# Kernel optimization log

Measured on AMD Instinct MI355X. Metric: run time of the kernel, lower is better.

## Reference

```python
import jax, jax.numpy as jnp
import numpy as np

B, L, S, H, E = 4, 1024, 1024, 8, 64


def setup_inputs() -> dict:
    key = jax.random.key(0)
    ks = jax.random.split(key, 8)
    return {
        "query": jax.random.normal(ks[0], (B, L, H, E), dtype=jnp.float32),
        "key": jax.random.normal(ks[1], (B, S, H, E), dtype=jnp.float32),
        "value": jax.random.normal(ks[2], (B, S, H, E), dtype=jnp.float32),
        "phi": jax.random.normal(ks[3], (H, L, S), dtype=jnp.float32),
        "log_gain": jnp.asarray(np.log(10.0), dtype=jnp.float32),
        "log_tau": jnp.asarray(np.log(2.0), dtype=jnp.float32),
        "log_tau_comm": jnp.asarray(np.log(0.2), dtype=jnp.float32),
        "hard_mask": jax.random.uniform(ks[4], (L, S), dtype=jnp.float32),
        "u": jax.random.uniform(ks[5], (H, L, S), dtype=jnp.float32),
        "mask_miss_k": jnp.ones((B, S), dtype=jnp.float32),
        "mask_miss_q": jnp.ones((B, L), dtype=jnp.float32),
        "pos": jnp.zeros((B, L), dtype=jnp.float32),
        "causal_mask": 0,
    }


def reference(query, key, value, phi, log_gain, log_tau, log_tau_comm,
              hard_mask, u, mask_miss_k, mask_miss_q, pos, causal_mask):
    # mask_miss_k/q, pos, causal_mask are unused by LieAttention.forward (torch parity)
    E_dim = query.shape[-1]
    scale = 1.0 / float(np.sqrt(E_dim))
    # raw scores (B, H, L, S)
    scores = jnp.einsum('blhe,bshe->bhls', query, key)
    # antisymmetric communication term
    comm = scores - jnp.swapaxes(scores, -1, -2)
    gain = jnp.clip(jnp.exp(log_gain), 1e-3, 1000.0)      # max_gain = 1000
    tau_comm = jnp.clip(jnp.exp(log_tau_comm), 1e-3, 10.0)
    comm_amp = jnp.tanh((gain / tau_comm) * comm)
    att = scale * jax.nn.gelu(comm_amp, approximate=False)  # torch F.gelu = exact erf
    # Gumbel-sigmoid relaxed DAG mask, broadcast over batch: M (1, H, L, S)
    tau = jnp.clip(jnp.exp(log_tau), 0.1, 5.0)             # tau_min/tau_max
    m_relaxed = jax.nn.sigmoid((jnp.log(u + 1e-8) - jnp.log(1.0 - u + 1e-8) + phi) / tau)
    att = att * m_relaxed[None]
    # hard mask (L, S) -> (1, 1, L, S)
    att = att * hard_mask[None, None]
    # attention entropy per query position: (B, H, L)
    eps = 1e-8
    entropy = jnp.nan_to_num(-jnp.sum(att * jnp.log(jnp.maximum(att, eps)), axis=-1))
    A = jnp.nan_to_num(att)  # dropout=0.0 -> identity
    V = jnp.einsum('bhls,bshd->blhd', A, value)
    return V, A, entropy
```

## Files before the change

### kernel.cpp

```cpp
#include <hip/hip_runtime.h>
#include <math.h>

#define Bn 4
#define Ln 1024
#define Sn 1024
#define Hn 8
#define En 64

typedef __attribute__((ext_vector_type(4))) float f32x4;
typedef __attribute__((ext_vector_type(8))) _Float16 h16x8;
typedef __attribute__((ext_vector_type(4))) _Float16 h16x4;

__device__ __forceinline__ float frcp(float x) { return __builtin_amdgcn_rcpf(x); }
__device__ __forceinline__ float fexp2(float x) {
    float r; asm("v_exp_f32 %0, %1" : "=v"(r) : "v"(x)); return r;
}
__device__ __forceinline__ float flog2(float x) {
    float r; asm("v_log_f32 %0, %1" : "=v"(r) : "v"(x)); return r;
}

__global__ __launch_bounds__(256) void prep(
    const float* __restrict__ Q, const float* __restrict__ K,
    const float* __restrict__ V,
    _Float16* __restrict__ Qh, _Float16* __restrict__ Ql,
    _Float16* __restrict__ Kh, _Float16* __restrict__ Kl,
    _Float16* __restrict__ Vt) {
    __shared__ float vlds[64][69];
    const int st = blockIdx.x;
    const int bh = blockIdx.y;
    const int b = bh >> 3, h = bh & 7;
    const int tid = threadIdx.x;
    const int s0 = st * 64;

#pragma unroll
    for (int i = 0; i < 4; ++i) {
        int idx = tid + 256 * i;
        int r = idx >> 4;
        int c4 = (idx & 15) << 2;
        size_t gin = (((size_t)b * Ln + s0 + r) * Hn + h) * En + c4;
        f32x4 qv = *(const f32x4*)(Q + gin);
        f32x4 kv = *(const f32x4*)(K + gin);
        f32x4 vv = *(const f32x4*)(V + gin);
        vlds[r][c4 + 0] = vv.x; vlds[r][c4 + 1] = vv.y;
        vlds[r][c4 + 2] = vv.z; vlds[r][c4 + 3] = vv.w;
        h16x4 qh4, ql4, kh4, kl4;
#pragma unroll
        for (int j = 0; j < 4; ++j) {
            float x = qv[j];
            _Float16 hx = (_Float16)x;
            qh4[j] = hx; ql4[j] = (_Float16)(x - (float)hx);
            float y = kv[j];
            _Float16 hy = (_Float16)y;
            kh4[j] = hy; kl4[j] = (_Float16)(y - (float)hy);
        }
        size_t ob = ((((size_t)bh * 16 + st) * 8 + (c4 >> 3)) * 64 + r) * 8 + (c4 & 7);
        *(h16x4*)(Qh + ob) = qh4; *(h16x4*)(Ql + ob) = ql4;
        *(h16x4*)(Kh + ob) = kh4; *(h16x4*)(Kl + ob) = kl4;
    }
    __syncthreads();
#pragma unroll
    for (int i = 0; i < 4; ++i) {
        int idx = tid + 256 * i;
        int d = idx >> 4;
        int sg = (idx & 15) << 2;
        h16x4 v4;
#pragma unroll
        for (int j = 0; j < 4; ++j) v4[j] = (_Float16)vlds[sg + j][d];
        size_t ob = ((((size_t)bh * 16 + st) * 8 + (sg >> 3)) * 64 + d) * 8 + (sg & 7);
        *(h16x4*)(Vt + ob) = v4;
    }
}

__global__ __launch_bounds__(256) void prep2(
    const float* __restrict__ phi, const float* __restrict__ u,
    const float* __restrict__ hard, const float* __restrict__ p_lt,
    _Float16* __restrict__ mh) {
    const float tau = fminf(fmaxf(expf(p_lt[0]), 0.1f), 5.0f);
    const float itau = 1.0f / tau;
    const size_t base = ((size_t)blockIdx.x * 256 + threadIdx.x) * 8;
    const size_t ls = base & (size_t)(Ln * Sn - 1);
    f32x4 ph0 = *(const f32x4*)(phi + base);
    f32x4 ph1 = *(const f32x4*)(phi + base + 4);
    f32x4 uu0 = *(const f32x4*)(u + base);
    f32x4 uu1 = *(const f32x4*)(u + base + 4);
    f32x4 hm0 = *(const f32x4*)(hard + ls);
    f32x4 hm1 = *(const f32x4*)(hard + ls + 4);
    h16x8 o;
#pragma unroll
    for (int j = 0; j < 4; ++j) {
        float z = (__logf((uu0[j] + 1e-8f) * frcp(1.0f - uu0[j] + 1e-8f)) + ph0[j]) * itau;
        float m = frcp(1.0f + __expf(-z));
        o[j] = (_Float16)(0.125f * m * hm0[j]);
    }
#pragma unroll
    for (int j = 0; j < 4; ++j) {
        float z = (__logf((uu1[j] + 1e-8f) * frcp(1.0f - uu1[j] + 1e-8f)) + ph1[j]) * itau;
        float m = frcp(1.0f + __expf(-z));
        o[4 + j] = (_Float16)(0.125f * m * hm1[j]);
    }
    *(h16x8*)(mh + base) = o;
}

__global__ __launch_bounds__(256, 4) void fused_lie(
    const _Float16* __restrict__ Qh, const _Float16* __restrict__ Ql,
    const _Float16* __restrict__ Kh, const _Float16* __restrict__ Kl,
    const _Float16* __restrict__ Vt, const _Float16* __restrict__ mh,
    const float* __restrict__ p_lg, const float* __restrict__ p_ltc,
    float* __restrict__ Aout, float* __restrict__ Vout,
    float* __restrict__ entOut) {
    __shared__ __align__(16) _Float16 plds[4][16 * 72];

    const int f = blockIdx.x;
    const int work = (f & 7) * 256 + (f >> 3);
    const int h = work >> 8;
    const int rem = work & 255;
    const int b = rem >> 6;
    const int tile = rem & 63;
    const int lt = tile >> 2;
    const int sq = tile & 3;
    const int bh = b * Hn + h;
    const int tid = threadIdx.x;
    const int w = tid >> 6;
    const int lane = tid & 63;
    const int q = lane >> 4;
    const int n = lane & 15;
    const int l0 = lt * 64;

    const float gain = fminf(fmaxf(expf(p_lg[0]), 1e-3f), 1000.0f);
    const float tauc = fminf(fmaxf(expf(p_ltc[0]), 1e-3f), 10.0f);
    const float c2l = 2.0f * gain / tauc * 1.44269504f;

    h16x8 QAh[2], QAl[2], KAh[2], KAl[2];
    {
        const size_t ab = (((size_t)bh * 16 + lt) * 8) * 512 + (size_t)(w * 16 + n) * 8;
#pragma unroll
        for (int kh = 0; kh < 2; ++kh) {
            size_t off = ab + (size_t)(q + 4 * kh) * 512;
            QAh[kh] = *(const h16x8*)(Qh + off);
            QAl[kh] = *(const h16x8*)(Ql + off);
            KAh[kh] = *(const h16x8*)(Kh + off);
            KAl[kh] = *(const h16x8*)(Kl + off);
        }
    }

    f32x4 accV[4];
#pragma unroll
    for (int i = 0; i < 4; ++i) accV[i] = (f32x4){0.f, 0.f, 0.f, 0.f};
    float entp[4] = {0.f, 0.f, 0.f, 0.f};

    const int lbase = l0 + w * 16 + q * 4;
    float* __restrict__ arow = Aout + (((size_t)b * Hn + h) * Ln + lbase) * (size_t)Sn;
    const _Float16* __restrict__ ment = mh + ((size_t)h * Ln + lbase) * (size_t)Sn;

    for (int stc = 0; stc < 4; ++stc) {
        const int st = sq * 4 + stc;
        const int s0 = st * 64;
        const size_t tb = (((size_t)bh * 16 + st) * 8) * 512;

        f32x4 a1[4], a2[4];
#pragma unroll
        for (int i = 0; i < 4; ++i) {
            a1[i] = (f32x4){0.f, 0.f, 0.f, 0.f};
            a2[i] = (f32x4){0.f, 0.f, 0.f, 0.f};
        }
#pragma unroll
        for (int kh = 0; kh < 2; ++kh) {
            const size_t kqb = tb + (size_t)(q + 4 * kh) * 512;
#pragma unroll
            for (int sub = 0; sub < 4; ++sub) {
                const size_t off = kqb + (size_t)(sub * 16 + n) * 8;
                h16x8 KBh = *(const h16x8*)(Kh + off);
                h16x8 KBl = *(const h16x8*)(Kl + off);
                h16x8 QBh = *(const h16x8*)(Qh + off);
                h16x8 QBl = *(const h16x8*)(Ql + off);
                f32x4 x1 = a1[sub], x2 = a2[sub];
                x1 = __builtin_amdgcn_mfma_f32_16x16x32_f16(QAh[kh], KBh, x1, 0, 0, 0);
                x1 = __builtin_amdgcn_mfma_f32_16x16x32_f16(QAh[kh], KBl, x1, 0, 0, 0);
                x1 = __builtin_amdgcn_mfma_f32_16x16x32_f16(QAl[kh], KBh, x1, 0, 0, 0);
                x2 = __builtin_amdgcn_mfma_f32_16x16x32_f16(KAh[kh], QBh, x2, 0, 0, 0);
                x2 = __builtin_amdgcn_mfma_f32_16x16x32_f16(KAh[kh], QBl, x2, 0, 0, 0);
                x2 = __builtin_amdgcn_mfma_f32_16x16x32_f16(KAl[kh], QBh, x2, 0, 0, 0);
                a1[sub] = x1; a2[sub] = x2;
            }
        }

#pragma unroll
        for (int sub = 0; sub < 4; ++sub) {
            const int s = s0 + sub * 16 + n;
#pragma unroll
            for (int r = 0; r < 4; ++r) {
                float mhv = (float)ment[(size_t)r * Sn + s];
                float cm = a1[sub][r] - a2[sub][r];
                float x = 1.0f - 2.0f * frcp(fexp2(c2l * cm) + 1.0f);
                float t = x * fmaf(0.044715f * x, x, 1.0f);
                float g = x * frcp(1.0f + fexp2(-2.30221271f * t));
                float att = g * mhv;
                arow[(size_t)r * Sn + s] = att;
                entp[r] += att * flog2(fmaxf(att, 1e-8f));
                plds[w][(q * 4 + r) * 72 + sub * 16 + n] = (_Float16)att;
            }
        }
        asm volatile("" ::: "memory");

        {
            const _Float16* pw = &plds[w][0];
#pragma unroll
            for (int kh = 0; kh < 2; ++kh) {
                const size_t kqb = tb + (size_t)(q + 4 * kh) * 512;
                h16x8 Pf = *(const h16x8*)&pw[n * 72 + q * 8 + kh * 32];
#pragma unroll
                for (int sub = 0; sub < 4; ++sub) {
                    h16x8 Vf = *(const h16x8*)(Vt + kqb + (size_t)(sub * 16 + n) * 8);
                    accV[sub] = __builtin_amdgcn_mfma_f32_16x16x32_f16(Pf, Vf, accV[sub], 0, 0, 0);
                }
            }
        }
        asm volatile("" ::: "memory");
    }

#pragma unroll
    for (int sub = 0; sub < 4; ++sub) {
#pragma unroll
        for (int r = 0; r < 4; ++r) {
            const int l = l0 + w * 16 + q * 4 + r;
            atomicAdd(Vout + (((size_t)b * Ln + l) * Hn + h) * En + sub * 16 + n, accV[sub][r]);
        }
    }
#pragma unroll
    for (int r = 0; r < 4; ++r) {
        float v = entp[r];
        v += __shfl_xor(v, 1);
        v += __shfl_xor(v, 2);
        v += __shfl_xor(v, 4);
        v += __shfl_xor(v, 8);
        if (n == 0) {
            atomicAdd(entOut + ((size_t)b * Hn + h) * Ln + lbase + r, -v * 0.69314718f);
        }
    }
}

extern "C" void kernel_launch(void* const* d_in, const int* in_sizes, int n_in,
                              void* d_out, int out_size, void* d_ws, size_t ws_size,
                              hipStream_t stream) {
    (void)in_sizes; (void)n_in; (void)ws_size; (void)out_size;

    const float* Q    = (const float*)d_in[0];
    const float* K    = (const float*)d_in[1];
    const float* Vv   = (const float*)d_in[2];
    const float* phi  = (const float*)d_in[3];
    const float* lg   = (const float*)d_in[4];
    const float* ltau = (const float*)d_in[5];
    const float* ltc  = (const float*)d_in[6];
    const float* hard = (const float*)d_in[7];
    const float* u    = (const float*)d_in[8];

    float* out  = (float*)d_out;
    float* Vout = out;
    float* Aout = out + (size_t)Bn * Ln * Hn * En;
    float* ent  = Aout + (size_t)Bn * Hn * Ln * Sn;

    const size_t NE = (size_t)32 * 1024 * 64;
    _Float16* Qh = (_Float16*)d_ws;
    _Float16* Ql = Qh + NE;
    _Float16* Kh = Ql + NE;
    _Float16* Kl = Kh + NE;
    _Float16* Vt = Kl + NE;
    _Float16* mh = Vt + NE;

    hipMemsetAsync(Vout, 0, (size_t)Bn * Ln * Hn * En * sizeof(float), stream);
    hipMemsetAsync(ent, 0, (size_t)Bn * Hn * Ln * sizeof(float), stream);
    prep<<<dim3(16, 32), 256, 0, stream>>>(Q, K, Vv, Qh, Ql, Kh, Kl, Vt);
    prep2<<<dim3(4096), 256, 0, stream>>>(phi, u, hard, ltau, mh);
    fused_lie<<<dim3(2048), 256, 0, stream>>>(Qh, Ql, Kh, Kl, Vt, mh,
                                              lg, ltc, Aout, Vout, ent);
}
```

Baseline: 366.1 us.

## Fold output zeroing into prep, split prep blocks, interleave score MFMAs with epilogue

Drops the two hipMemsetAsync calls and instead zeroes Vout and the entropy buffer inside the prep kernel, which now runs four times as many blocks, each converting 16 rows instead of 64. In the fused kernel, each 16-column sub-tile's score MFMAs are followed directly by its activation epilogue instead of computing all sub-tiles first, which lowers register pressure and lets MFMA work overlap with the transcendental math. The large attention-matrix stores become nontemporal to avoid polluting cache. The risks are a different instruction schedule and more small prep blocks.

```diff
diff --git a/kernel.cpp b/kernel.cpp
--- a/kernel.cpp
+++ b/kernel.cpp
@@ -24,25 +24,33 @@
     const float* __restrict__ V,
     _Float16* __restrict__ Qh, _Float16* __restrict__ Ql,
     _Float16* __restrict__ Kh, _Float16* __restrict__ Kl,
-    _Float16* __restrict__ Vt) {
-    __shared__ float vlds[64][69];
-    const int st = blockIdx.x;
+    _Float16* __restrict__ Vt, float* __restrict__ Vout,
+    float* __restrict__ entOut) {
+    __shared__ float vlds[16][69];
+    const int bx = blockIdx.x;
+    const int st = bx >> 2;
+    const int rg = bx & 3;
     const int bh = blockIdx.y;
     const int b = bh >> 3, h = bh & 7;
     const int tid = threadIdx.x;
     const int s0 = st * 64;
 
-#pragma unroll
-    for (int i = 0; i < 4; ++i) {
-        int idx = tid + 256 * i;
-        int r = idx >> 4;
-        int c4 = (idx & 15) << 2;
-        size_t gin = (((size_t)b * Ln + s0 + r) * Hn + h) * En + c4;
+    {
+        const int flat = (blockIdx.y * 64 + bx) * 256 + tid;
+        *(f32x4*)(Vout + (size_t)flat * 4) = (f32x4){0.f, 0.f, 0.f, 0.f};
+        if (flat < 8192) *(f32x4*)(entOut + (size_t)flat * 4) = (f32x4){0.f, 0.f, 0.f, 0.f};
+    }
+
+    {
+        const int r16 = tid >> 4;
+        const int c4 = (tid & 15) << 2;
+        const int row = rg * 16 + r16;
+        size_t gin = (((size_t)b * Ln + s0 + row) * Hn + h) * En + c4;
         f32x4 qv = *(const f32x4*)(Q + gin);
         f32x4 kv = *(const f32x4*)(K + gin);
         f32x4 vv = *(const f32x4*)(V + gin);
-        vlds[r][c4 + 0] = vv.x; vlds[r][c4 + 1] = vv.y;
-        vlds[r][c4 + 2] = vv.z; vlds[r][c4 + 3] = vv.w;
+        vlds[r16][c4 + 0] = vv.x; vlds[r16][c4 + 1] = vv.y;
+        vlds[r16][c4 + 2] = vv.z; vlds[r16][c4 + 3] = vv.w;
         h16x4 qh4, ql4, kh4, kl4;
 #pragma unroll
         for (int j = 0; j < 4; ++j) {
@@ -53,19 +61,18 @@
             _Float16 hy = (_Float16)y;
             kh4[j] = hy; kl4[j] = (_Float16)(y - (float)hy);
         }
-        size_t ob = ((((size_t)bh * 16 + st) * 8 + (c4 >> 3)) * 64 + r) * 8 + (c4 & 7);
+        size_t ob = ((((size_t)bh * 16 + st) * 8 + (c4 >> 3)) * 64 + row) * 8 + (c4 & 7);
         *(h16x4*)(Qh + ob) = qh4; *(h16x4*)(Ql + ob) = ql4;
         *(h16x4*)(Kh + ob) = kh4; *(h16x4*)(Kl + ob) = kl4;
     }
     __syncthreads();
-#pragma unroll
-    for (int i = 0; i < 4; ++i) {
-        int idx = tid + 256 * i;
-        int d = idx >> 4;
-        int sg = (idx & 15) << 2;
+    {
+        const int d = tid >> 2;
+        const int sgl = (tid & 3) << 2;
         h16x4 v4;
 #pragma unroll
-        for (int j = 0; j < 4; ++j) v4[j] = (_Float16)vlds[sg + j][d];
+        for (int j = 0; j < 4; ++j) v4[j] = (_Float16)vlds[sgl + j][d];
+        const int sg = rg * 16 + sgl;
         size_t ob = ((((size_t)bh * 16 + st) * 8 + (sg >> 3)) * 64 + d) * 8 + (sg & 7);
         *(h16x4*)(Vt + ob) = v4;
     }
@@ -157,45 +164,34 @@
         const int s0 = st * 64;
         const size_t tb = (((size_t)bh * 16 + st) * 8) * 512;
 
-        f32x4 a1[4], a2[4];
-#pragma unroll
-        for (int i = 0; i < 4; ++i) {
-            a1[i] = (f32x4){0.f, 0.f, 0.f, 0.f};
-            a2[i] = (f32x4){0.f, 0.f, 0.f, 0.f};
-        }
-#pragma unroll
-        for (int kh = 0; kh < 2; ++kh) {
-            const size_t kqb = tb + (size_t)(q + 4 * kh) * 512;
-#pragma unroll
-            for (int sub = 0; sub < 4; ++sub) {
-                const size_t off = kqb + (size_t)(sub * 16 + n) * 8;
+#pragma unroll
+        for (int sub = 0; sub < 4; ++sub) {
+            f32x4 x1 = (f32x4){0.f, 0.f, 0.f, 0.f};
+            f32x4 x2 = (f32x4){0.f, 0.f, 0.f, 0.f};
+#pragma unroll
+            for (int kh = 0; kh < 2; ++kh) {
+                const size_t off = tb + (size_t)(q + 4 * kh) * 512 + (size_t)(sub * 16 + n) * 8;
                 h16x8 KBh = *(const h16x8*)(Kh + off);
                 h16x8 KBl = *(const h16x8*)(Kl + off);
                 h16x8 QBh = *(const h16x8*)(Qh + off);
                 h16x8 QBl = *(const h16x8*)(Ql + off);
-                f32x4 x1 = a1[sub], x2 = a2[sub];
                 x1 = __builtin_amdgcn_mfma_f32_16x16x32_f16(QAh[kh], KBh, x1, 0, 0, 0);
                 x1 = __builtin_amdgcn_mfma_f32_16x16x32_f16(QAh[kh], KBl, x1, 0, 0, 0);
                 x1 = __builtin_amdgcn_mfma_f32_16x16x32_f16(QAl[kh], KBh, x1, 0, 0, 0);
                 x2 = __builtin_amdgcn_mfma_f32_16x16x32_f16(KAh[kh], QBh, x2, 0, 0, 0);
                 x2 = __builtin_amdgcn_mfma_f32_16x16x32_f16(KAh[kh], QBl, x2, 0, 0, 0);
                 x2 = __builtin_amdgcn_mfma_f32_16x16x32_f16(KAl[kh], QBh, x2, 0, 0, 0);
-                a1[sub] = x1; a2[sub] = x2;
             }
-        }
-
-#pragma unroll
-        for (int sub = 0; sub < 4; ++sub) {
             const int s = s0 + sub * 16 + n;
 #pragma unroll
             for (int r = 0; r < 4; ++r) {
                 float mhv = (float)ment[(size_t)r * Sn + s];
-                float cm = a1[sub][r] - a2[sub][r];
+                float cm = x1[r] - x2[r];
                 float x = 1.0f - 2.0f * frcp(fexp2(c2l * cm) + 1.0f);
                 float t = x * fmaf(0.044715f * x, x, 1.0f);
                 float g = x * frcp(1.0f + fexp2(-2.30221271f * t));
                 float att = g * mhv;
-                arow[(size_t)r * Sn + s] = att;
+                __builtin_nontemporal_store(att, &arow[(size_t)r * Sn + s]);
                 entp[r] += att * flog2(fmaxf(att, 1e-8f));
                 plds[w][(q * 4 + r) * 72 + sub * 16 + n] = (_Float16)att;
             }
@@ -267,9 +263,7 @@
     _Float16* Vt = Kl + NE;
     _Float16* mh = Vt + NE;
 
-    hipMemsetAsync(Vout, 0, (size_t)Bn * Ln * Hn * En * sizeof(float), stream);
-    hipMemsetAsync(ent, 0, (size_t)Bn * Hn * Ln * sizeof(float), stream);
-    prep<<<dim3(16, 32), 256, 0, stream>>>(Q, K, Vv, Qh, Ql, Kh, Kl, Vt);
+    prep<<<dim3(64, 32), 256, 0, stream>>>(Q, K, Vv, Qh, Ql, Kh, Kl, Vt, Vout, ent);
     prep2<<<dim3(4096), 256, 0, stream>>>(phi, u, hard, ltau, mh);
     fused_lie<<<dim3(2048), 256, 0, stream>>>(Qh, Ql, Kh, Kl, Vt, mh,
                                               lg, ltc, Aout, Vout, ent);
```

Measured after the change: 389.7 us. +6.4%, slower.
